# Optimization experiments

Hardware: AMD Instinct MI355X
Metric: run time of the kernel (lower is better)

## Reference

```python
import jax, jax.numpy as jnp
import numpy as np

B, L, D, O = 4, 2048, 4096, 4096   # batch, seq, in_features, out_features
P = 2                               # n_pack
NF = 2000                           # n_frequency
NFP = NF // P                       # frequencies per pack
IN_P, OUT_P = D // P, O // P        # per-pack spectrum grid
NGATE = P * D // 10                 # gate parameter count
SCALING = 150.0


def setup_inputs() -> dict:
    key = jax.random.key(0)
    ks = jax.random.split(key, 6)
    x = jax.random.normal(ks[0], (B, L, D), dtype=jnp.float32)
    base_w = jax.random.normal(ks[1], (O, D), dtype=jnp.float32) * 0.02
    base_b = jax.random.normal(ks[2], (O,), dtype=jnp.float32) * 0.02
    spectrum = jax.random.normal(ks[3], (P, NFP), dtype=jnp.float32)
    B_list = jax.random.normal(ks[4], (P, P, P), dtype=jnp.float32) * 0.5
    gate_param = jax.random.normal(ks[5], (NGATE,), dtype=jnp.float32)
    # unique random frequency locations per pack (mirrors torch.randperm)
    rng = np.random.default_rng(777)
    idx = jnp.asarray(np.stack([rng.permutation(OUT_P * IN_P)[:NFP] for _ in range(P)]), dtype=jnp.int64)
    gidx = jnp.asarray(rng.permutation(P * D)[:NGATE], dtype=jnp.int64)
    return {"x": x, "base_w": base_w, "base_b": base_b, "spectrum": spectrum,
            "B_list": B_list, "gate_param": gate_param, "idx": idx, "gidx": gidx}


def _delta_weight(spec_i, idx_i, B_i, dtype):
    # scatter sparse spectrum into (OUT_P, IN_P) grid
    dense = jnp.zeros((OUT_P, IN_P), dtype).at[idx_i // IN_P, idx_i % IN_P].set(spec_i)
    A = jnp.fft.ifft2(dense).real  # (OUT_P, IN_P)
    # kron(A, B_i) -> (O, D)
    return SCALING * (A[:, None, :, None] * B_i[None, :, None, :]).reshape(O, D)


def reference(x, base_w, base_b, spectrum, B_list, gate_param, idx, gidx):
    dt = x.dtype
    # base linear
    result = jnp.einsum('bld,od->blo', x, base_w) + base_b
    # gate matrix: scatter then ifft2
    gate_m = jnp.zeros((P, D), dt).at[gidx // D, gidx % D].set(gate_param)
    gate_m = jnp.fft.ifft2(gate_m).real  # (P, D)
    gate_w = jax.nn.softmax(jnp.einsum('bld,ed->ble', x, gate_m), axis=-1)  # (B,L,P)
    # per-pack delta weights and outputs
    deltas = jax.vmap(lambda s, i, b: _delta_weight(s, i, b, dt))(spectrum, idx, B_list)  # (P,O,D)
    outputs = jnp.einsum('bld,pod->blpo', x, deltas)  # (B,L,P,O)
    final = jnp.einsum('blpo,blp->blo', outputs, gate_w)
    return (result + final).astype(dt)
```

## Files before the change

kernel.cpp:

```cpp
#include <hip/hip_runtime.h>


#define AS1 __attribute__((address_space(1)))
#define AS3 __attribute__((address_space(3)))

using bf16x8   = __attribute__((ext_vector_type(8))) __bf16;
using f32x4    = __attribute__((ext_vector_type(4))) float;
using ushort8v = __attribute__((ext_vector_type(8))) unsigned short;
using ushort4v = __attribute__((ext_vector_type(4))) unsigned short;

__device__ __forceinline__ unsigned short f2bf(float f) {
  unsigned int u = __float_as_uint(f);
  u += 0x7FFFu + ((u >> 16) & 1u);
  return (unsigned short)(u >> 16);
}

__device__ __forceinline__ void gll16(void* lds, const void* g) {
  __builtin_amdgcn_global_load_lds((AS1 void*)(g), (AS3 void*)(lds), 16, 0, 0);
}

__global__ void k_gatem(const float* __restrict__ gp, const int* __restrict__ gidx,
                        float* __restrict__ gatem, int NG) {
  int t = blockIdx.x * 256 + threadIdx.x;
  int e = t >> 12, d = t & 4095;
  float acc = 0.f;
  for (int k = 0; k < NG; k++) {
    int iv = gidx[k];
    int dk = iv & 4095;
    float th = (float)((d * dk) & 4095) * 1.5339807878856412e-3f;
    float cv = __cosf(th);
    float v = gp[k] * cv;
    acc += ((e & (iv >> 12)) & 1) ? -v : v;
  }
  gatem[t] = acc * (1.f / 8192.f);
}

__global__ void k_tables(const float* __restrict__ spec, const int* __restrict__ idx,
                         unsigned short* __restrict__ tbl, int NFP) {
  int z = blockIdx.y;
  int p = z >> 1, isQ = z & 1;
  int t = blockIdx.x * 256 + threadIdx.x;
  int r = t >> 11, kk = t & 2047;
  unsigned short v = 0;
  if (kk < 2 * NFP) {
    int j = (kk < NFP) ? kk : kk - NFP;
    int iv = idx[p * NFP + j];
    int f = isQ ? (iv & 2047) : (iv >> 11);
    float th = (float)((r * f) & 2047) * 3.0679615757712823e-3f;
    float val = (kk < NFP) ? __cosf(th) : __sinf(th);
    if (isQ) {
      float s = spec[p * NFP + j];
      val *= (kk < NFP) ? s : -s;
    }
    v = f2bf(val);
  }
  tbl[(size_t)z * 4194304 + t] = v;
}

__global__ void k_gate(const float* __restrict__ x, const float* __restrict__ gatem,
                       float* __restrict__ g) {
  int n = blockIdx.x * 4 + (threadIdx.x >> 6);
  int l = threadIdx.x & 63;
  const float4* xr  = (const float4*)(x + (size_t)n * 4096);
  const float4* g0p = (const float4*)(gatem);
  const float4* g1p = (const float4*)(gatem + 4096);
  float s0 = 0.f, s1 = 0.f;
  for (int t = 0; t < 16; t++) {
    int ii = l + (t << 6);
    float4 xv = xr[ii], a = g0p[ii], b = g1p[ii];
    s0 += xv.x * a.x + xv.y * a.y + xv.z * a.z + xv.w * a.w;
    s1 += xv.x * b.x + xv.y * b.y + xv.z * b.z + xv.w * b.w;
  }
  for (int off = 32; off > 0; off >>= 1) {
    s0 += __shfl_down(s0, off);
    s1 += __shfl_down(s1, off);
  }
  if (l == 0) {
    float mx = fmaxf(s0, s1);
    float e0 = __expf(s0 - mx), e1 = __expf(s1 - mx);
    float inv = 1.f / (e0 + e1);
    g[2 * n] = e0 * inv;
    g[2 * n + 1] = e1 * inv;
  }
}

__global__ void k_convx(const float* __restrict__ x, unsigned short* __restrict__ xb,
                        unsigned short* __restrict__ Zg, const float* __restrict__ Bl,
                        const float* __restrict__ g) {
  size_t t = (size_t)blockIdx.x * 256 + threadIdx.x;
  const float4* xp = (const float4*)x + t * 2;
  float4 v0 = xp[0], v1 = xp[1];
  ushort8v xv;
  xv[0]=f2bf(v0.x); xv[1]=f2bf(v0.y); xv[2]=f2bf(v0.z); xv[3]=f2bf(v0.w);
  xv[4]=f2bf(v1.x); xv[5]=f2bf(v1.y); xv[6]=f2bf(v1.z); xv[7]=f2bf(v1.w);
  *(ushort8v*)(xb + t * 8) = xv;
  int n = (int)(t >> 9);
  int c0 = ((int)t & 511) * 4;
  float gg[2] = {g[2 * n], g[2 * n + 1]};
  float xe[4] = {v0.x, v0.z, v1.x, v1.z};
  float xo[4] = {v0.y, v0.w, v1.y, v1.w};
  #pragma unroll
  for (int pa = 0; pa < 4; pa++) {
    int p = pa >> 1, a = pa & 1;
    float b0 = Bl[pa * 2] * gg[p], b1 = Bl[pa * 2 + 1] * gg[p];
    ushort4v yv;
    #pragma unroll
    for (int c = 0; c < 4; c++) yv[c] = f2bf(b0 * xe[c] + b1 * xo[c]);
    *(ushort4v*)(Zg + (size_t)a * 33554432 + (size_t)n * 4096 + p * 2048 + c0) = yv;
  }
}

__global__ void k_convw(const float* __restrict__ w, unsigned short* __restrict__ wb) {
  size_t t = (size_t)blockIdx.x * 256 + threadIdx.x;
  const float4* sp = (const float4*)w + t * 2;
  float4 v0 = sp[0], v1 = sp[1];
  ushort8v o;
  o[0]=f2bf(v0.x); o[1]=f2bf(v0.y); o[2]=f2bf(v0.z); o[3]=f2bf(v0.w);
  o[4]=f2bf(v1.x); o[5]=f2bf(v1.y); o[6]=f2bf(v1.z); o[7]=f2bf(v1.w);
  *(ushort8v*)(wb + t * 8) = o;
}

__device__ __forceinline__ void gemm_core(
    const unsigned short* __restrict__ Amat, int lda,
    const unsigned short* __restrict__ Bmat, int ldb,
    int K, char* As, char* Bs, f32x4 acc[4][4]) {
  const int tid = threadIdx.x;
  const int w = tid >> 6, l = tid & 63;
  const int quad = l >> 4, l15 = l & 15;
  const int wm = (w >> 1) << 6, wn = (w & 1) << 6;

  int c1 = (w << 6) + l, c2 = c1 + 256;
  int r1 = c1 >> 2, q1 = (c1 & 3) ^ ((r1 >> 1) & 3);
  int r2 = c2 >> 2, q2 = (c2 & 3) ^ ((r2 >> 1) & 3);
  const unsigned short* aS1 = Amat + (size_t)r1 * lda + (q1 << 3);
  const unsigned short* aS2 = Amat + (size_t)r2 * lda + (q2 << 3);
  const unsigned short* bS1 = Bmat + (size_t)r1 * ldb + (q1 << 3);
  const unsigned short* bS2 = Bmat + (size_t)r2 * ldb + (q2 << 3);
  char* aD1 = As + (w << 10);
  char* aD2 = As + 4096 + (w << 10);
  char* bD1 = Bs + (w << 10);
  char* bD2 = Bs + 4096 + (w << 10);

  int aOff[4], bOff[4];
  #pragma unroll
  for (int i = 0; i < 4; i++) {
    int ra = wm + (i << 4) + l15;
    aOff[i] = (ra << 6) + ((quad ^ ((ra >> 1) & 3)) << 4);
    int rb = wn + (i << 4) + l15;
    bOff[i] = (rb << 6) + ((quad ^ ((rb >> 1) & 3)) << 4);
  }

  for (int kt = 0; kt < K; kt += 32) {
    __syncthreads();
    gll16(aD1, aS1); gll16(aD2, aS2);
    gll16(bD1, bS1); gll16(bD2, bS2);
    __syncthreads();
    bf16x8 af[4], bfv[4];
    #pragma unroll
    for (int i = 0; i < 4; i++) af[i]  = *(const bf16x8*)(As + aOff[i]);
    #pragma unroll
    for (int j = 0; j < 4; j++) bfv[j] = *(const bf16x8*)(Bs + bOff[j]);
    #pragma unroll
    for (int i = 0; i < 4; i++)
      #pragma unroll
      for (int j = 0; j < 4; j++)
        acc[i][j] = __builtin_amdgcn_mfma_f32_16x16x32_bf16(af[i], bfv[j], acc[i][j], 0, 0, 0);
    aS1 += 32; aS2 += 32; bS1 += 32; bS2 += 32;
  }
}

__global__ __launch_bounds__(256, 2) void k_abuild(
    const unsigned short* __restrict__ tbl, unsigned short* __restrict__ Acat) {
  __shared__ __align__(16) char sm[16384];
  const int p = blockIdx.z;
  const unsigned short* P = tbl + (size_t)(2 * p) * 4194304;
  const unsigned short* Q = tbl + (size_t)(2 * p + 1) * 4194304;
  f32x4 acc[4][4];
  #pragma unroll
  for (int i = 0; i < 4; i++)
    #pragma unroll
    for (int j = 0; j < 4; j++) acc[i][j] = (f32x4){0.f, 0.f, 0.f, 0.f};
  const int m0 = blockIdx.x << 7, n0 = blockIdx.y << 7;
  gemm_core(P + (size_t)m0 * 2048, 2048, Q + (size_t)n0 * 2048, 2048, 2048,
            sm, sm + 8192, acc);
  const int tid = threadIdx.x, w = tid >> 6, l = tid & 63;
  const int quad = l >> 4, l15 = l & 15;
  const int wm = (w >> 1) << 6, wn = (w & 1) << 6;
  const float SC = 150.f / 4194304.f;
  unsigned short* Ap = Acat + (size_t)p * 2048;
  #pragma unroll
  for (int j = 0; j < 4; j++) {
    int c = n0 + wn + (j << 4) + l15;
    #pragma unroll
    for (int i = 0; i < 4; i++) {
      int rb = m0 + wm + (i << 4) + (quad << 2);
      #pragma unroll
      for (int reg = 0; reg < 4; reg++)
        Ap[(size_t)(rb + reg) * 4096 + c] = f2bf(acc[i][j][reg] * SC);
    }
  }
}


__device__ __forceinline__ void stg_unit(char* sm, const unsigned short* base,
                                         size_t soff, int wid, int buf, int isb,
                                         int kt) {
  char* d = sm + buf * 32768 + isb * 16384 + (wid << 10);
  gll16(d,        base + soff + kt);
  gll16(d + 8192, base + soff + 524288 + kt);
}

__device__ __forceinline__ void tile_step(
    char* sm, const unsigned short* __restrict__ Ap,
    const unsigned short* __restrict__ Bp, size_t soff,
    int aB, int bB, int wid, f32x4 (&acc)[8][4], int T, bool do_stg, int vm) {
  bf16x8 af[8], bfv[4];
  char* bb = sm + (T & 3) * 32768;
  af[0] = *(const bf16x8*)(bb + aB);
  #pragma unroll
  for (int j = 0; j < 4; j++) bfv[j] = *(const bf16x8*)(bb + bB + j * 1024);
  #pragma unroll
  for (int i = 1; i < 8; i++) af[i] = *(const bf16x8*)(bb + aB + i * 1024);
  if (do_stg) {
    stg_unit(sm, Ap, soff, wid, (T + 3) & 3, 0, (T + 3) << 5);
    stg_unit(sm, Bp, soff, wid, (T + 3) & 3, 1, (T + 3) << 5);
  }
  __builtin_amdgcn_s_setprio(1);
  #pragma unroll
  for (int i = 0; i < 8; i++)
    #pragma unroll
    for (int j = 0; j < 4; j++)
      acc[i][j] = __builtin_amdgcn_mfma_f32_16x16x32_bf16(af[i], bfv[j], acc[i][j], 0, 0, 0);
  __builtin_amdgcn_s_setprio(0);
  if (vm == 8)      asm volatile("s_waitcnt vmcnt(8) lgkmcnt(0)" ::: "memory");
  else if (vm == 4) asm volatile("s_waitcnt vmcnt(4) lgkmcnt(0)" ::: "memory");
  else              asm volatile("s_waitcnt vmcnt(0) lgkmcnt(0)" ::: "memory");
  __builtin_amdgcn_s_barrier();
}

__device__ __forceinline__ void gemm256(const unsigned short* __restrict__ Ap,
                                        const unsigned short* __restrict__ Bp,
                                        char* sm, f32x4 (&acc)[8][4]) {
  const int tid = threadIdx.x;
  const int wid = tid >> 6, lane = tid & 63;
  const int quad = lane >> 4, l15 = lane & 15;
  const int wr = wid >> 2, wc = wid & 3;
  const int srow = tid >> 2, g = tid & 3;
  const int q = g ^ ((srow >> 1) & 3);
  const size_t soff = (size_t)srow * 4096 + (size_t)(q << 3);
  const int slotx = (quad ^ ((l15 >> 1) & 3)) << 4;
  const int aB = (((wr << 7) + l15) << 6) + slotx;
  const int bB = (((wc << 6) + l15) << 6) + slotx + 16384;

  stg_unit(sm, Ap, soff, wid, 0, 0, 0);
  stg_unit(sm, Bp, soff, wid, 0, 1, 0);
  stg_unit(sm, Ap, soff, wid, 1, 0, 32);
  stg_unit(sm, Bp, soff, wid, 1, 1, 32);
  stg_unit(sm, Ap, soff, wid, 2, 0, 64);
  stg_unit(sm, Bp, soff, wid, 2, 1, 64);
  asm volatile("s_waitcnt vmcnt(8)" ::: "memory");
  __builtin_amdgcn_s_barrier();

  #pragma unroll 4
  for (int t = 0; t < 125; t++)
    tile_step(sm, Ap, Bp, soff, aB, bB, wid, acc, t, true, 8);
  tile_step(sm, Ap, Bp, soff, aB, bB, wid, acc, 125, false, 4);
  tile_step(sm, Ap, Bp, soff, aB, bB, wid, acc, 126, false, 0);
  tile_step(sm, Ap, Bp, soff, aB, bB, wid, acc, 127, false, 0);
}

__global__ __launch_bounds__(512, 1) void k_base(
    const unsigned short* __restrict__ xb, const unsigned short* __restrict__ wb,
    const float* __restrict__ bias, float* __restrict__ out) {
  __shared__ __align__(16) char sm[131072];
  int lid = blockIdx.x + (blockIdx.y << 4);
  int nl = ((lid & 7) << 6) + (lid >> 3);
  const int m0 = (nl >> 4) << 8, n0 = (nl & 15) << 8;
  f32x4 acc[8][4];
  #pragma unroll
  for (int i = 0; i < 8; i++)
    #pragma unroll
    for (int j = 0; j < 4; j++) acc[i][j] = (f32x4){0.f, 0.f, 0.f, 0.f};
  gemm256(xb + (size_t)m0 * 4096, wb + (size_t)n0 * 4096, sm, acc);
  const int tid = threadIdx.x, wid = tid >> 6, lane = tid & 63;
  const int quad = lane >> 4, l15 = lane & 15;
  const int wr = wid >> 2, wc = wid & 3;
  #pragma unroll
  for (int j = 0; j < 4; j++) {
    int o = n0 + (wc << 6) + (j << 4) + l15;
    float bv = bias[o];
    #pragma unroll
    for (int i = 0; i < 8; i++) {
      int mb = m0 + (wr << 7) + (i << 4) + (quad << 2);
      #pragma unroll
      for (int reg = 0; reg < 4; reg++)
        out[(size_t)(mb + reg) * 4096 + o] = acc[i][j][reg] + bv;
    }
  }
}

__global__ __launch_bounds__(512, 1) void k_pack(
    const unsigned short* __restrict__ Zg, const unsigned short* __restrict__ Acat,
    float* __restrict__ out) {
  __shared__ __align__(16) char sm[131072];
  int lid = blockIdx.x + (blockIdx.y << 3);
  int nl = ((lid & 7) << 6) + (lid >> 3);
  const int bx = nl & 7, by = nl >> 3;
  const int a = by & 1, nt = by >> 1;
  const int r0 = bx << 8;
  f32x4 acc[8][4];
  #pragma unroll
  for (int i = 0; i < 8; i++)
    #pragma unroll
    for (int j = 0; j < 4; j++) acc[i][j] = (f32x4){0.f, 0.f, 0.f, 0.f};
  gemm256(Zg + ((size_t)(a << 13) + (size_t)(nt << 8)) * 4096,
          Acat + (size_t)r0 * 4096, sm, acc);
  const int tid = threadIdx.x, wid = tid >> 6, lane = tid & 63;
  const int quad = lane >> 4, l15 = lane & 15;
  const int wr = wid >> 2, wc = wid & 3;
  #pragma unroll
  for (int j = 0; j < 4; j++) {
    int r = r0 + (wc << 6) + (j << 4) + l15;
    #pragma unroll
    for (int i = 0; i < 8; i++) {
      int nb = (nt << 8) + (wr << 7) + (i << 4) + (quad << 2);
      #pragma unroll
      for (int reg = 0; reg < 4; reg++) {
        float* p = out + (size_t)(nb + reg) * 4096 + 2 * r + a;
        *p += acc[i][j][reg];
      }
    }
  }
}

extern "C" void kernel_launch(void* const* d_in, const int* in_sizes, int n_in,
                              void* d_out, int out_size, void* d_ws, size_t ws_size,
                              hipStream_t stream) {
  const float* x    = (const float*)d_in[0];
  const float* basw = (const float*)d_in[1];
  const float* basb = (const float*)d_in[2];
  const float* spec = (const float*)d_in[3];
  const float* Bl   = (const float*)d_in[4];
  const float* gp   = (const float*)d_in[5];
  const int*   idx  = (const int*)d_in[6];
  const int*   gidx = (const int*)d_in[7];
  const int NFP = in_sizes[3] / 2;
  const int NG  = in_sizes[5];

  char* ws = (char*)d_ws;
  float*          gbuf  = (float*)(ws);
  float*          gatem = (float*)(ws + (64ull << 10));
  unsigned short* Acat  = (unsigned short*)(ws + (1ull << 20));
  unsigned short* xb    = (unsigned short*)(ws + (32ull << 20));
  unsigned short* bwb   = (unsigned short*)(ws + (96ull << 20));
  unsigned short* Zg    = (unsigned short*)(ws + (128ull << 20));
  unsigned short* tbl   = (unsigned short*)(ws + (128ull << 20));
  float* outp = (float*)d_out;

  k_gatem <<<32, 256, 0, stream>>>(gp, gidx, gatem, NG);
  k_tables<<<dim3(16384, 4), 256, 0, stream>>>(spec, idx, tbl, NFP);
  k_abuild<<<dim3(16, 16, 2), 256, 0, stream>>>(tbl, Acat);
  k_gate  <<<2048, 256, 0, stream>>>(x, gatem, gbuf);
  k_convx <<<16384, 256, 0, stream>>>(x, xb, Zg, Bl, gbuf);
  k_convw <<<8192, 256, 0, stream>>>(basw, bwb);
  k_base  <<<dim3(16, 32), 512, 0, stream>>>(xb, bwb, basb, outp);
  k_pack  <<<dim3(8, 64), 512, 0, stream>>>(Zg, Acat, outp);
  (void)n_in; (void)out_size; (void)ws_size;
}
```

Baseline: 1.001 ms.

## Pipeline k_abuild GEMM with 4-stage LDS ring and larger 128x256 tiles

Rewrites the spectrum-build GEMM kernel (k_abuild) to use 512-thread blocks computing 128x256 tiles, with a four-buffer LDS ring that prefetches three K-steps ahead via global_load_lds. Partial vmcnt waits and one barrier per step replace the two __syncthreads per K-step of the old loop, and MFMA issue gets raised priority. The aim is to hide global-load latency and cut synchronisation in this precomputation GEMM. In exchange it uses 96KB of LDS, which allows only one block per CU.

```diff
diff --git a/kernel.cpp b/kernel.cpp
--- a/kernel.cpp
+++ b/kernel.cpp
@@ -120,87 +120,6 @@
   *(ushort8v*)(wb + t * 8) = o;
 }
 
-__device__ __forceinline__ void gemm_core(
-    const unsigned short* __restrict__ Amat, int lda,
-    const unsigned short* __restrict__ Bmat, int ldb,
-    int K, char* As, char* Bs, f32x4 acc[4][4]) {
-  const int tid = threadIdx.x;
-  const int w = tid >> 6, l = tid & 63;
-  const int quad = l >> 4, l15 = l & 15;
-  const int wm = (w >> 1) << 6, wn = (w & 1) << 6;
-
-  int c1 = (w << 6) + l, c2 = c1 + 256;
-  int r1 = c1 >> 2, q1 = (c1 & 3) ^ ((r1 >> 1) & 3);
-  int r2 = c2 >> 2, q2 = (c2 & 3) ^ ((r2 >> 1) & 3);
-  const unsigned short* aS1 = Amat + (size_t)r1 * lda + (q1 << 3);
-  const unsigned short* aS2 = Amat + (size_t)r2 * lda + (q2 << 3);
-  const unsigned short* bS1 = Bmat + (size_t)r1 * ldb + (q1 << 3);
-  const unsigned short* bS2 = Bmat + (size_t)r2 * ldb + (q2 << 3);
-  char* aD1 = As + (w << 10);
-  char* aD2 = As + 4096 + (w << 10);
-  char* bD1 = Bs + (w << 10);
-  char* bD2 = Bs + 4096 + (w << 10);
-
-  int aOff[4], bOff[4];
-  #pragma unroll
-  for (int i = 0; i < 4; i++) {
-    int ra = wm + (i << 4) + l15;
-    aOff[i] = (ra << 6) + ((quad ^ ((ra >> 1) & 3)) << 4);
-    int rb = wn + (i << 4) + l15;
-    bOff[i] = (rb << 6) + ((quad ^ ((rb >> 1) & 3)) << 4);
-  }
-
-  for (int kt = 0; kt < K; kt += 32) {
-    __syncthreads();
-    gll16(aD1, aS1); gll16(aD2, aS2);
-    gll16(bD1, bS1); gll16(bD2, bS2);
-    __syncthreads();
-    bf16x8 af[4], bfv[4];
-    #pragma unroll
-    for (int i = 0; i < 4; i++) af[i]  = *(const bf16x8*)(As + aOff[i]);
-    #pragma unroll
-    for (int j = 0; j < 4; j++) bfv[j] = *(const bf16x8*)(Bs + bOff[j]);
-    #pragma unroll
-    for (int i = 0; i < 4; i++)
-      #pragma unroll
-      for (int j = 0; j < 4; j++)
-        acc[i][j] = __builtin_amdgcn_mfma_f32_16x16x32_bf16(af[i], bfv[j], acc[i][j], 0, 0, 0);
-    aS1 += 32; aS2 += 32; bS1 += 32; bS2 += 32;
-  }
-}
-
-__global__ __launch_bounds__(256, 2) void k_abuild(
-    const unsigned short* __restrict__ tbl, unsigned short* __restrict__ Acat) {
-  __shared__ __align__(16) char sm[16384];
-  const int p = blockIdx.z;
-  const unsigned short* P = tbl + (size_t)(2 * p) * 4194304;
-  const unsigned short* Q = tbl + (size_t)(2 * p + 1) * 4194304;
-  f32x4 acc[4][4];
-  #pragma unroll
-  for (int i = 0; i < 4; i++)
-    #pragma unroll
-    for (int j = 0; j < 4; j++) acc[i][j] = (f32x4){0.f, 0.f, 0.f, 0.f};
-  const int m0 = blockIdx.x << 7, n0 = blockIdx.y << 7;
-  gemm_core(P + (size_t)m0 * 2048, 2048, Q + (size_t)n0 * 2048, 2048, 2048,
-            sm, sm + 8192, acc);
-  const int tid = threadIdx.x, w = tid >> 6, l = tid & 63;
-  const int quad = l >> 4, l15 = l & 15;
-  const int wm = (w >> 1) << 6, wn = (w & 1) << 6;
-  const float SC = 150.f / 4194304.f;
-  unsigned short* Ap = Acat + (size_t)p * 2048;
-  #pragma unroll
-  for (int j = 0; j < 4; j++) {
-    int c = n0 + wn + (j << 4) + l15;
-    #pragma unroll
-    for (int i = 0; i < 4; i++) {
-      int rb = m0 + wm + (i << 4) + (quad << 2);
-      #pragma unroll
-      for (int reg = 0; reg < 4; reg++)
-        Ap[(size_t)(rb + reg) * 4096 + c] = f2bf(acc[i][j][reg] * SC);
-    }
-  }
-}
-
 
 __device__ __forceinline__ void stg_unit(char* sm, const unsigned short* base,
                                          size_t soff, int wid, int buf, int isb,
@@ -269,6 +188,97 @@
   tile_step(sm, Ap, Bp, soff, aB, bB, wid, acc, 127, false, 0);
 }
 
+
+__device__ __forceinline__ void abuild_tile(
+    char* sm, const unsigned short* __restrict__ Pp,
+    const unsigned short* __restrict__ Qp, size_t soff,
+    int aB, int bB, int wid, f32x4 (&acc)[4][4], int T, bool do_stg, int vm) {
+  bf16x8 af[4], bfv[4];
+  char* bb = sm + (T & 3) * 24576;
+  af[0] = *(const bf16x8*)(bb + aB);
+  #pragma unroll
+  for (int j = 0; j < 4; j++) bfv[j] = *(const bf16x8*)(bb + bB + j * 1024);
+  #pragma unroll
+  for (int i = 1; i < 4; i++) af[i] = *(const bf16x8*)(bb + aB + i * 1024);
+  if (do_stg) {
+    const int buf = (T + 3) & 3, kt = (T + 3) << 5;
+    char* d = sm + buf * 24576;
+    gll16(d + (wid << 10),        Pp + soff + kt);
+    gll16(d + 8192 + (wid << 10), Qp + soff + kt);
+    gll16(d + 16384 + (wid << 10), Qp + soff + 262144 + kt);
+  }
+  __builtin_amdgcn_s_setprio(1);
+  #pragma unroll
+  for (int i = 0; i < 4; i++)
+    #pragma unroll
+    for (int j = 0; j < 4; j++)
+      acc[i][j] = __builtin_amdgcn_mfma_f32_16x16x32_bf16(af[i], bfv[j], acc[i][j], 0, 0, 0);
+  __builtin_amdgcn_s_setprio(0);
+  if (vm == 6)      asm volatile("s_waitcnt vmcnt(6) lgkmcnt(0)" ::: "memory");
+  else if (vm == 3) asm volatile("s_waitcnt vmcnt(3) lgkmcnt(0)" ::: "memory");
+  else              asm volatile("s_waitcnt vmcnt(0) lgkmcnt(0)" ::: "memory");
+  __builtin_amdgcn_s_barrier();
+}
+
+__global__ __launch_bounds__(512, 1) void k_abuild(
+    const unsigned short* __restrict__ tbl, unsigned short* __restrict__ Acat) {
+  __shared__ __align__(16) char sm[98304];
+  const int p = blockIdx.z;
+  const int m0 = blockIdx.x << 7;
+  const int n0 = blockIdx.y << 8;
+  const unsigned short* Pp = tbl + (size_t)(2 * p) * 4194304 + (size_t)m0 * 2048;
+  const unsigned short* Qp = tbl + (size_t)(2 * p + 1) * 4194304 + (size_t)n0 * 2048;
+
+  const int tid = threadIdx.x;
+  const int wid = tid >> 6, lane = tid & 63;
+  const int quad = lane >> 4, l15 = lane & 15;
+  const int wr = wid >> 2, wc = wid & 3;
+  const int srow = tid >> 2, g = tid & 3;
+  const int q = g ^ ((srow >> 1) & 3);
+  const size_t soff = (size_t)srow * 2048 + (size_t)(q << 3);
+  const int slotx = (quad ^ ((l15 >> 1) & 3)) << 4;
+  const int aB = (((wr << 6) + l15) << 6) + slotx;
+  const int bB = (((wc << 6) + l15) << 6) + slotx + 8192;
+
+  f32x4 acc[4][4];
+  #pragma unroll
+  for (int i = 0; i < 4; i++)
+    #pragma unroll
+    for (int j = 0; j < 4; j++) acc[i][j] = (f32x4){0.f, 0.f, 0.f, 0.f};
+
+  #pragma unroll
+  for (int t0 = 0; t0 < 3; t0++) {
+    char* d = sm + t0 * 24576;
+    const int kt = t0 << 5;
+    gll16(d + (wid << 10),         Pp + soff + kt);
+    gll16(d + 8192 + (wid << 10),  Qp + soff + kt);
+    gll16(d + 16384 + (wid << 10), Qp + soff + 262144 + kt);
+  }
+  asm volatile("s_waitcnt vmcnt(6)" ::: "memory");
+  __builtin_amdgcn_s_barrier();
+
+  #pragma unroll 4
+  for (int t = 0; t < 61; t++)
+    abuild_tile(sm, Pp, Qp, soff, aB, bB, wid, acc, t, true, 6);
+  abuild_tile(sm, Pp, Qp, soff, aB, bB, wid, acc, 61, false, 3);
+  abuild_tile(sm, Pp, Qp, soff, aB, bB, wid, acc, 62, false, 0);
+  abuild_tile(sm, Pp, Qp, soff, aB, bB, wid, acc, 63, false, 0);
+
+  const float SC = 150.f / 4194304.f;
+  unsigned short* Ap = Acat + (size_t)p * 2048;
+  #pragma unroll
+  for (int j = 0; j < 4; j++) {
+    int c = n0 + (wc << 6) + (j << 4) + l15;
+    #pragma unroll
+    for (int i = 0; i < 4; i++) {
+      int rb = m0 + (wr << 6) + (i << 4) + (quad << 2);
+      #pragma unroll
+      for (int reg = 0; reg < 4; reg++)
+        Ap[(size_t)(rb + reg) * 4096 + c] = f2bf(acc[i][j][reg] * SC);
+    }
+  }
+}
+
 __global__ __launch_bounds__(512, 1) void k_base(
     const unsigned short* __restrict__ xb, const unsigned short* __restrict__ wb,
     const float* __restrict__ bias, float* __restrict__ out) {
@@ -359,7 +369,7 @@
 
   k_gatem <<<32, 256, 0, stream>>>(gp, gidx, gatem, NG);
   k_tables<<<dim3(16384, 4), 256, 0, stream>>>(spec, idx, tbl, NFP);
-  k_abuild<<<dim3(16, 16, 2), 256, 0, stream>>>(tbl, Acat);
+  k_abuild<<<dim3(16, 8, 2), 512, 0, stream>>>(tbl, Acat);
   k_gate  <<<2048, 256, 0, stream>>>(x, gatem, gbuf);
   k_convx <<<16384, 256, 0, stream>>>(x, xb, Zg, Bl, gbuf);
   k_convw <<<8192, 256, 0, stream>>>(basw, bwb);
```

Result: no change. 995.5 us (-0.6%).
